# Optimization experiments

Measured on AMD Instinct MI355X. Metric: run time of the kernel, lower is better.

The kernel has to match this reference:

```python
import jax, jax.numpy as jnp
import numpy as np

B, T, D_IN, D_H, D_OUT = 32, 1024, 512, 1024, 512

def setup_inputs() -> dict:
    key = jax.random.key(0)
    kx, k1, k2, k3, k4, k5, k6 = jax.random.split(key, 7)
    # scale weights like typical init (1/sqrt(fan_in)) so sigmoid stays in a sane range
    x = jax.random.normal(kx, (B, T, D_IN), dtype=jnp.float32)
    Wh_w = jax.random.normal(k1, (D_H, D_H), dtype=jnp.float32) / np.sqrt(D_H)
    Wh_b = jax.random.normal(k2, (D_H,), dtype=jnp.float32) * 0.01
    Wx_w = jax.random.normal(k3, (D_H, D_IN), dtype=jnp.float32) / np.sqrt(D_IN)
    Wx_b = jax.random.normal(k4, (D_H,), dtype=jnp.float32) * 0.01
    Wy_w = jax.random.normal(k5, (D_OUT, D_H), dtype=jnp.float32) / np.sqrt(D_H)
    Wy_b = jax.random.normal(k6, (D_OUT,), dtype=jnp.float32) * 0.01
    return {"x": x, "Wh_w": Wh_w, "Wh_b": Wh_b, "Wx_w": Wx_w, "Wx_b": Wx_b,
            "Wy_w": Wy_w, "Wy_b": Wy_b}

def reference(x, Wh_w, Wh_b, Wx_w, Wx_b, Wy_w, Wy_b):
    # h_t = sigmoid(Wh h_{t-1} + b_h + Wx x_t + b_x); y_t = Wy h_t + b_y
    # Precompute input projection for all timesteps (one big GEMM).
    xp = jnp.einsum('bti,hi->bth', x, Wx_w) + Wx_b + Wh_b  # [B,T,H]
    xp_t = jnp.swapaxes(xp, 0, 1)  # [T,B,H] for scan
    h0 = jnp.zeros((x.shape[0], Wh_w.shape[0]), dtype=x.dtype)

    def step(h, xpt):
        h = jax.nn.sigmoid(h @ Wh_w.T + xpt)  # [B,H]
        y = h @ Wy_w.T + Wy_b                 # [B,O]
        return h, y

    _, ys = jax.lax.scan(step, h0, xp_t)  # ys: [T,B,O]
    return jnp.swapaxes(ys, 0, 1)  # [B,T,O]
```

## Files before the change

kernel.cpp:

```cpp
#include <hip/hip_runtime.h>

constexpr int Bb = 32;
constexpr int Tt = 1024;
constexpr int Hh = 1024;
constexpr int Di = 512;
constexpr int Do = 512;

using bf16x8 = __attribute__((ext_vector_type(8))) short;
using f32x4  = __attribute__((ext_vector_type(4))) float;

__device__ __forceinline__ f32x4 mfma16(bf16x8 a, bf16x8 b, f32x4 c) {
  return __builtin_amdgcn_mfma_f32_16x16x32_bf16(a, b, c, 0, 0, 0);
}
__device__ __forceinline__ unsigned short f2bf(float f) {
  unsigned u = __builtin_bit_cast(unsigned, f);
  u += 0x7FFFu + ((u >> 16) & 1u);
  return (unsigned short)(u >> 16);
}
__device__ __forceinline__ float bf2f(unsigned short h) {
  unsigned u = ((unsigned)h) << 16;
  return __builtin_bit_cast(float, u);
}

__device__ __forceinline__ void llc_store_u16(void* p, unsigned v) {
  asm volatile("global_store_short %0, %1, off sc0 sc1" :: "v"(p), "v"(v) : "memory");
}
__device__ __forceinline__ void llc_store_u32(void* p, unsigned v) {
  asm volatile("global_store_dword %0, %1, off sc0 sc1" :: "v"(p), "v"(v) : "memory");
}
__device__ __forceinline__ uint4 llc_load_flags(const void* p) {
  uint4 r;
  asm volatile("global_load_dwordx4 %0, %1, off sc0 sc1\n\ts_waitcnt vmcnt(0)"
               : "=v"(r) : "v"(p) : "memory");
  return r;
}

__global__ __launch_bounds__(256) void cvt4_kernel(const float* __restrict__ s,
                                                   unsigned short* __restrict__ d) {
  int i = (blockIdx.x * 256 + threadIdx.x) * 4;
  float4 v = *(const float4*)(s + i);
  ushort4 u = { f2bf(v.x), f2bf(v.y), f2bf(v.z), f2bf(v.w) };
  *(ushort4*)(d + i) = u;
}

template <int MODE>
__global__ __launch_bounds__(256)
void gemm_kernel(const void* __restrict__ Ap, const float* __restrict__ Bw,
                 const float* __restrict__ bias1, const float* __restrict__ bias2,
                 void* __restrict__ Cp) {
  constexpr int K = (MODE == 0) ? Di : Hh;
  constexpr int BM = 64, BN = 64, BK = 64;
  __shared__ unsigned short As[BM][80];
  __shared__ unsigned short Bs[BN][80];

  const int m0 = blockIdx.x * BM;
  const int n0 = blockIdx.y * BN;
  const int tid = threadIdx.x;
  const int lane = tid & 63;
  const int wave = tid >> 6;
  const int wm = (wave & 1) * 32;
  const int wn = (wave >> 1) * 32;
  const int fr = lane & 15;
  const int kg = lane >> 4;

  f32x4 acc[2][2] = {};

  const int srow = tid >> 2;
  const int scb  = (tid & 3) * 16;

  for (int k0 = 0; k0 < K; k0 += BK) {
    if constexpr (MODE == 0) {
      const float* a = (const float*)Ap + (size_t)(m0 + srow) * K + k0 + scb;
#pragma unroll
      for (int q = 0; q < 4; ++q) {
        float4 v = ((const float4*)a)[q];
        ushort4 u = { f2bf(v.x), f2bf(v.y), f2bf(v.z), f2bf(v.w) };
        *(ushort4*)&As[srow][scb + q * 4] = u;
      }
    } else {
      const unsigned short* a = (const unsigned short*)Ap + (size_t)(m0 + srow) * K + k0 + scb;
      *(uint4*)&As[srow][scb]     = ((const uint4*)a)[0];
      *(uint4*)&As[srow][scb + 8] = ((const uint4*)a)[1];
    }
    {
      const float* b = Bw + (size_t)(n0 + srow) * K + k0 + scb;
#pragma unroll
      for (int q = 0; q < 4; ++q) {
        float4 v = ((const float4*)b)[q];
        ushort4 u = { f2bf(v.x), f2bf(v.y), f2bf(v.z), f2bf(v.w) };
        *(ushort4*)&Bs[srow][scb + q * 4] = u;
      }
    }
    __syncthreads();

#pragma unroll
    for (int kk = 0; kk < 2; ++kk) {
      const int kb = kk * 32 + kg * 8;
      bf16x8 af[2], bf[2];
      af[0] = *(const bf16x8*)&As[wm + fr][kb];
      af[1] = *(const bf16x8*)&As[wm + 16 + fr][kb];
      bf[0] = *(const bf16x8*)&Bs[wn + fr][kb];
      bf[1] = *(const bf16x8*)&Bs[wn + 16 + fr][kb];
#pragma unroll
      for (int i = 0; i < 2; ++i)
#pragma unroll
        for (int j = 0; j < 2; ++j)
          acc[i][j] = mfma16(af[i], bf[j], acc[i][j]);
    }
    __syncthreads();
  }

#pragma unroll
  for (int i = 0; i < 2; ++i) {
#pragma unroll
    for (int j = 0; j < 2; ++j) {
      const int n = n0 + wn + j * 16 + fr;
      float bv;
      if constexpr (MODE == 0) bv = bias1[n] + bias2[n];
      else                     bv = bias1[n];
#pragma unroll
      for (int q = 0; q < 4; ++q) {
        const int m = m0 + wm + i * 16 + kg * 4 + q;
        float v = acc[i][j][q] + bv;
        if constexpr (MODE == 0) {
          int bb = m >> 10, ttt = m & 1023;
          ((unsigned short*)Cp)[((size_t)ttt * Bb + bb) * Hh + n] = f2bf(v);
        } else {
          int bb = m & 31, ttt = m >> 5;
          ((float*)Cp)[((size_t)bb * Tt + ttt) * Do + n] = v;
        }
      }
    }
  }
}

__global__ __launch_bounds__(512)
void scan_kernel(const unsigned short* __restrict__ Whb,
                 const unsigned short* __restrict__ xp,
                 unsigned short* __restrict__ hist,
                 unsigned short* __restrict__ hbuf,
                 unsigned* __restrict__ flags) {
  __shared__ unsigned short panel[16 * 1024];

  const int tid = threadIdx.x;
  const int g = blockIdx.x >> 3;
  const int r = blockIdx.x & 7;
  const int wave = tid >> 6;
  const int lane = tid & 63;
  const int nloc = lane & 15;
  const int kgrp = lane >> 4;
  const int hrow = r * 128 + wave * 16 + nloc;
  const int gb0 = g * 16;
  const int xmask = (nloc & 7) << 3;

  bf16x8 wf[32];
  {
    const unsigned short* wb = Whb + (size_t)hrow * Hh + kgrp * 8;
#pragma unroll
    for (int kk = 0; kk < 32; ++kk) wf[kk] = *(const bf16x8*)(wb + kk * 32);
#pragma unroll
    for (int kk = 0; kk < 32; ++kk) asm volatile("" : "+v"(wf[kk]));
  }

  unsigned* gflags = flags + g * 64;
  const int sb  = tid >> 5;
  const int sk0 = (tid & 31) * 32;

  for (int t = 0; t < Tt; ++t) {
    const int par = t & 1;
    const unsigned short* hsrc = hbuf + (size_t)par * Bb * Hh;
    unsigned short* hdst = hbuf + (size_t)(par ^ 1) * Bb * Hh;

    unsigned short xpv[4];
    const size_t xb = (size_t)t * Bb * Hh + hrow;
#pragma unroll
    for (int i = 0; i < 4; ++i) xpv[i] = xp[xb + (size_t)(gb0 + kgrp * 4 + i) * Hh];

    if (tid == 0) {
      for (;;) {
        uint4 f0 = llc_load_flags(gflags);
        uint4 f1 = llc_load_flags(gflags + 4);
        unsigned mn = f0.x;
        mn = mn < f0.y ? mn : f0.y;  mn = mn < f0.z ? mn : f0.z;  mn = mn < f0.w ? mn : f0.w;
        mn = mn < f1.x ? mn : f1.x;  mn = mn < f1.y ? mn : f1.y;
        mn = mn < f1.z ? mn : f1.z;  mn = mn < f1.w ? mn : f1.w;
        if (mn >= (unsigned)t) break;
      }
    }
    __syncthreads();

    {
      const unsigned* gsrc = (const unsigned*)(hsrc + (size_t)(gb0 + sb) * Hh + sk0);
      unsigned tmp[16];
#pragma unroll
      for (int q = 0; q < 16; ++q)
        tmp[q] = __hip_atomic_load(gsrc + q, __ATOMIC_RELAXED, __HIP_MEMORY_SCOPE_AGENT);
#pragma unroll
      for (int c = 0; c < 4; ++c) {
        uint4 v = { tmp[4 * c], tmp[4 * c + 1], tmp[4 * c + 2], tmp[4 * c + 3] };
        *(uint4*)&panel[sb * 1024 + ((sk0 + c * 8) ^ ((sb & 7) << 3))] = v;
      }
    }
    __syncthreads();

    f32x4 acc0 = {0.f, 0.f, 0.f, 0.f}, acc1 = {0.f, 0.f, 0.f, 0.f};
#pragma unroll
    for (int kk = 0; kk < 32; kk += 2) {
      bf16x8 a0 = *(const bf16x8*)&panel[nloc * 1024 + ((kk * 32 + kgrp * 8) ^ xmask)];
      bf16x8 a1 = *(const bf16x8*)&panel[nloc * 1024 + (((kk + 1) * 32 + kgrp * 8) ^ xmask)];
      acc0 = mfma16(a0, wf[kk], acc0);
      acc1 = mfma16(a1, wf[kk + 1], acc1);
    }
    f32x4 acc = acc0 + acc1;

    const size_t tb = (size_t)t * Bb * Hh;
#pragma unroll
    for (int i = 0; i < 4; ++i) {
      const int mb = gb0 + kgrp * 4 + i;
      float pre = acc[i] + bf2f(xpv[i]);
      float h = 1.0f / (1.0f + __expf(-pre));
      unsigned hb = f2bf(h);
      llc_store_u16(hdst + (size_t)mb * Hh + hrow, hb);
      hist[tb + (size_t)mb * Hh + hrow] = (unsigned short)hb;
    }

    asm volatile("s_waitcnt vmcnt(0)" ::: "memory");
    __syncthreads();
    if (tid == 0) llc_store_u32(gflags + r, (unsigned)(t + 1));
  }
}

extern "C" void kernel_launch(void* const* d_in, const int* in_sizes, int n_in,
                              void* d_out, int out_size, void* d_ws, size_t ws_size,
                              hipStream_t stream) {
  const float* x    = (const float*)d_in[0];
  const float* Wh_w = (const float*)d_in[1];
  const float* Wh_b = (const float*)d_in[2];
  const float* Wx_w = (const float*)d_in[3];
  const float* Wx_b = (const float*)d_in[4];
  const float* Wy_w = (const float*)d_in[5];
  const float* Wy_b = (const float*)d_in[6];

  char* ws = (char*)d_ws;
  constexpr size_t XP_OFF   = 0;
  constexpr size_t HIST_OFF = XP_OFF   + (size_t)Tt * Bb * Hh * 2;
  constexpr size_t WH_OFF   = HIST_OFF + (size_t)Tt * Bb * Hh * 2;
  constexpr size_t HBUF_OFF = WH_OFF   + (size_t)Hh * Hh * 2;
  constexpr size_t FLG_OFF  = HBUF_OFF + (size_t)2 * Bb * Hh * 2;

  unsigned short* xp   = (unsigned short*)(ws + XP_OFF);
  unsigned short* hist = (unsigned short*)(ws + HIST_OFF);
  unsigned short* whb  = (unsigned short*)(ws + WH_OFF);
  unsigned short* hbuf = (unsigned short*)(ws + HBUF_OFF);
  unsigned*       flags = (unsigned*)(ws + FLG_OFF);

  hipMemsetAsync(ws + HBUF_OFF, 0, (size_t)2 * Bb * Hh * 2 + 512, stream);

  cvt4_kernel<<<dim3((Hh * Hh) / (256 * 4)), dim3(256), 0, stream>>>(Wh_w, whb);

  gemm_kernel<0><<<dim3((Bb * Tt) / 64, Hh / 64), dim3(256), 0, stream>>>(
      (const void*)x, Wx_w, Wx_b, Wh_b, (void*)xp);

  {
    void* sargs[5] = { (void*)&whb, (void*)&xp, (void*)&hist, (void*)&hbuf, (void*)&flags };
    hipLaunchCooperativeKernel((const void*)scan_kernel, dim3(16), dim3(512), sargs, 0, stream);
  }

  gemm_kernel<1><<<dim3((Bb * Tt) / 64, Do / 64), dim3(256), 0, stream>>>(
      (const void*)hist, Wy_w, Wy_b, nullptr, d_out);
}
```

Baseline: 7.148 ms.

## Replace flag-based step barrier with per-element tagged hidden-state words

The scan kernel drops the separate per-group flag array, where one thread polled and then the block synchronised. Each hidden value is now stored as a 32-bit word holding the timestep tag in the high half and the bf16 value in the low half, in a triple-buffered array. Consumer threads poll their own 128-byte slice until every tag matches the expected step, then unpack the values into shared memory. This removes the producer-side vmcnt wait, a block barrier and the flag round trip from each step's critical path, at the cost of doubling the bytes moved per hidden-state exchange.

```diff
diff --git a/kernel.cpp b/kernel.cpp
--- a/kernel.cpp
+++ b/kernel.cpp
@@ -5,6 +5,7 @@
 constexpr int Hh = 1024;
 constexpr int Di = 512;
 constexpr int Do = 512;
+constexpr int TGSZ = Bb * Hh;
 
 using bf16x8 = __attribute__((ext_vector_type(8))) short;
 using f32x4  = __attribute__((ext_vector_type(4))) float;
@@ -20,19 +21,6 @@
 __device__ __forceinline__ float bf2f(unsigned short h) {
   unsigned u = ((unsigned)h) << 16;
   return __builtin_bit_cast(float, u);
-}
-
-__device__ __forceinline__ void llc_store_u16(void* p, unsigned v) {
-  asm volatile("global_store_short %0, %1, off sc0 sc1" :: "v"(p), "v"(v) : "memory");
-}
-__device__ __forceinline__ void llc_store_u32(void* p, unsigned v) {
-  asm volatile("global_store_dword %0, %1, off sc0 sc1" :: "v"(p), "v"(v) : "memory");
-}
-__device__ __forceinline__ uint4 llc_load_flags(const void* p) {
-  uint4 r;
-  asm volatile("global_load_dwordx4 %0, %1, off sc0 sc1\n\ts_waitcnt vmcnt(0)"
-               : "=v"(r) : "v"(p) : "memory");
-  return r;
 }
 
 __global__ __launch_bounds__(256) void cvt4_kernel(const float* __restrict__ s,
@@ -41,6 +29,11 @@
   float4 v = *(const float4*)(s + i);
   ushort4 u = { f2bf(v.x), f2bf(v.y), f2bf(v.z), f2bf(v.w) };
   *(ushort4*)(d + i) = u;
+}
+
+__global__ __launch_bounds__(256) void init_tags(unsigned* __restrict__ tg) {
+  int i = blockIdx.x * 256 + threadIdx.x;
+  tg[i] = (i < TGSZ) ? 0xFFFF0000u : 0xEEEE0000u;
 }
 
 template <int MODE>
@@ -96,16 +89,16 @@
 #pragma unroll
     for (int kk = 0; kk < 2; ++kk) {
       const int kb = kk * 32 + kg * 8;
-      bf16x8 af[2], bf[2];
-      af[0] = *(const bf16x8*)&As[wm + fr][kb];
-      af[1] = *(const bf16x8*)&As[wm + 16 + fr][kb];
-      bf[0] = *(const bf16x8*)&Bs[wn + fr][kb];
-      bf[1] = *(const bf16x8*)&Bs[wn + 16 + fr][kb];
+      bf16x8 af[2], bfr[2];
+      af[0]  = *(const bf16x8*)&As[wm + fr][kb];
+      af[1]  = *(const bf16x8*)&As[wm + 16 + fr][kb];
+      bfr[0] = *(const bf16x8*)&Bs[wn + fr][kb];
+      bfr[1] = *(const bf16x8*)&Bs[wn + 16 + fr][kb];
 #pragma unroll
       for (int i = 0; i < 2; ++i)
 #pragma unroll
         for (int j = 0; j < 2; ++j)
-          acc[i][j] = mfma16(af[i], bf[j], acc[i][j]);
+          acc[i][j] = mfma16(af[i], bfr[j], acc[i][j]);
     }
     __syncthreads();
   }
@@ -138,8 +131,7 @@
 void scan_kernel(const unsigned short* __restrict__ Whb,
                  const unsigned short* __restrict__ xp,
                  unsigned short* __restrict__ hist,
-                 unsigned short* __restrict__ hbuf,
-                 unsigned* __restrict__ flags) {
+                 unsigned* __restrict__ tg) {
   __shared__ unsigned short panel[16 * 1024];
 
   const int tid = threadIdx.x;
@@ -158,48 +150,63 @@
     const unsigned short* wb = Whb + (size_t)hrow * Hh + kgrp * 8;
 #pragma unroll
     for (int kk = 0; kk < 32; ++kk) wf[kk] = *(const bf16x8*)(wb + kk * 32);
-#pragma unroll
-    for (int kk = 0; kk < 32; ++kk) asm volatile("" : "+v"(wf[kk]));
-  }
-
-  unsigned* gflags = flags + g * 64;
-  const int sb  = tid >> 5;
-  const int sk0 = (tid & 31) * 32;
+  }
+
+  const int sb  = tid & 15;
+  const int kc  = tid >> 4;
+  const int sxs = (sb & 7) << 3;
 
   for (int t = 0; t < Tt; ++t) {
-    const int par = t & 1;
-    const unsigned short* hsrc = hbuf + (size_t)par * Bb * Hh;
-    unsigned short* hdst = hbuf + (size_t)(par ^ 1) * Bb * Hh;
+#pragma unroll
+    for (int kk = 0; kk < 32; kk += 8)
+      asm volatile("" : "+v"(wf[kk]), "+v"(wf[kk + 1]), "+v"(wf[kk + 2]), "+v"(wf[kk + 3]),
+                        "+v"(wf[kk + 4]), "+v"(wf[kk + 5]), "+v"(wf[kk + 6]), "+v"(wf[kk + 7]));
+
+    const int par = t % 3;
+    const int nxt = (t + 1) % 3;
 
     unsigned short xpv[4];
     const size_t xb = (size_t)t * Bb * Hh + hrow;
 #pragma unroll
     for (int i = 0; i < 4; ++i) xpv[i] = xp[xb + (size_t)(gb0 + kgrp * 4 + i) * Hh];
 
-    if (tid == 0) {
-      for (;;) {
-        uint4 f0 = llc_load_flags(gflags);
-        uint4 f1 = llc_load_flags(gflags + 4);
-        unsigned mn = f0.x;
-        mn = mn < f0.y ? mn : f0.y;  mn = mn < f0.z ? mn : f0.z;  mn = mn < f0.w ? mn : f0.w;
-        mn = mn < f1.x ? mn : f1.x;  mn = mn < f1.y ? mn : f1.y;
-        mn = mn < f1.z ? mn : f1.z;  mn = mn < f1.w ? mn : f1.w;
-        if (mn >= (unsigned)t) break;
-      }
-    }
-    __syncthreads();
+    const unsigned exp = ((unsigned)t - 1u) & 0xFFFFu;
+    const unsigned* src = tg + (size_t)par * TGSZ + (size_t)(gb0 + sb) * Hh + kc * 32;
+    uint4 d0, d1, d2, d3, d4, d5, d6, d7;
+    unsigned bad;
+    do {
+      asm volatile(
+          "global_load_dwordx4 %0, %8, off sc0 sc1\n\t"
+          "global_load_dwordx4 %1, %8, off offset:16 sc0 sc1\n\t"
+          "global_load_dwordx4 %2, %8, off offset:32 sc0 sc1\n\t"
+          "global_load_dwordx4 %3, %8, off offset:48 sc0 sc1\n\t"
+          "global_load_dwordx4 %4, %8, off offset:64 sc0 sc1\n\t"
+          "global_load_dwordx4 %5, %8, off offset:80 sc0 sc1\n\t"
+          "global_load_dwordx4 %6, %8, off offset:96 sc0 sc1\n\t"
+          "global_load_dwordx4 %7, %8, off offset:112 sc0 sc1\n\t"
+          "s_waitcnt vmcnt(0)"
+          : "=v"(d0), "=v"(d1), "=v"(d2), "=v"(d3),
+            "=v"(d4), "=v"(d5), "=v"(d6), "=v"(d7)
+          : "v"(src) : "memory");
+      bad = 0;
+#define CHK(v) bad |= ((v.x >> 16) ^ exp) | ((v.y >> 16) ^ exp) | \
+                      ((v.z >> 16) ^ exp) | ((v.w >> 16) ^ exp)
+      CHK(d0); CHK(d1); CHK(d2); CHK(d3); CHK(d4); CHK(d5); CHK(d6); CHK(d7);
+#undef CHK
+    } while (bad);
 
     {
-      const unsigned* gsrc = (const unsigned*)(hsrc + (size_t)(gb0 + sb) * Hh + sk0);
-      unsigned tmp[16];
-#pragma unroll
-      for (int q = 0; q < 16; ++q)
-        tmp[q] = __hip_atomic_load(gsrc + q, __ATOMIC_RELAXED, __HIP_MEMORY_SCOPE_AGENT);
-#pragma unroll
-      for (int c = 0; c < 4; ++c) {
-        uint4 v = { tmp[4 * c], tmp[4 * c + 1], tmp[4 * c + 2], tmp[4 * c + 3] };
-        *(uint4*)&panel[sb * 1024 + ((sk0 + c * 8) ^ ((sb & 7) << 3))] = v;
-      }
+#define PK(a, b) (((a) & 0xFFFFu) | ((b) << 16))
+      uint4 p0 = { PK(d0.x, d0.y), PK(d0.z, d0.w), PK(d1.x, d1.y), PK(d1.z, d1.w) };
+      uint4 p1 = { PK(d2.x, d2.y), PK(d2.z, d2.w), PK(d3.x, d3.y), PK(d3.z, d3.w) };
+      uint4 p2 = { PK(d4.x, d4.y), PK(d4.z, d4.w), PK(d5.x, d5.y), PK(d5.z, d5.w) };
+      uint4 p3 = { PK(d6.x, d6.y), PK(d6.z, d6.w), PK(d7.x, d7.y), PK(d7.z, d7.w) };
+#undef PK
+      const int pb = sb * 1024, k0 = kc * 32;
+      *(uint4*)&panel[pb + ((k0)      ^ sxs)] = p0;
+      *(uint4*)&panel[pb + ((k0 + 8)  ^ sxs)] = p1;
+      *(uint4*)&panel[pb + ((k0 + 16) ^ sxs)] = p2;
+      *(uint4*)&panel[pb + ((k0 + 24) ^ sxs)] = p3;
     }
     __syncthreads();
 
@@ -214,19 +221,20 @@
     f32x4 acc = acc0 + acc1;
 
     const size_t tb = (size_t)t * Bb * Hh;
+    unsigned* dbase = tg + (size_t)nxt * TGSZ + hrow;
 #pragma unroll
     for (int i = 0; i < 4; ++i) {
       const int mb = gb0 + kgrp * 4 + i;
       float pre = acc[i] + bf2f(xpv[i]);
       float h = 1.0f / (1.0f + __expf(-pre));
-      unsigned hb = f2bf(h);
-      llc_store_u16(hdst + (size_t)mb * Hh + hrow, hb);
-      hist[tb + (size_t)mb * Hh + hrow] = (unsigned short)hb;
-    }
-
-    asm volatile("s_waitcnt vmcnt(0)" ::: "memory");
-    __syncthreads();
-    if (tid == 0) llc_store_u32(gflags + r, (unsigned)(t + 1));
+      unsigned short hb = f2bf(h);
+      unsigned word = ((unsigned)t << 16) | (unsigned)hb;
+      asm volatile("global_store_dword %0, %1, off sc0 sc1"
+                   :: "v"(dbase + (size_t)mb * Hh), "v"(word) : "memory");
+      hist[tb + (size_t)mb * Hh + hrow] = hb;
+    }
+
+    __syncthreads();
   }
 }
 
@@ -245,16 +253,14 @@
   constexpr size_t XP_OFF   = 0;
   constexpr size_t HIST_OFF = XP_OFF   + (size_t)Tt * Bb * Hh * 2;
   constexpr size_t WH_OFF   = HIST_OFF + (size_t)Tt * Bb * Hh * 2;
-  constexpr size_t HBUF_OFF = WH_OFF   + (size_t)Hh * Hh * 2;
-  constexpr size_t FLG_OFF  = HBUF_OFF + (size_t)2 * Bb * Hh * 2;
+  constexpr size_t TG_OFF   = WH_OFF   + (size_t)Hh * Hh * 2;
 
   unsigned short* xp   = (unsigned short*)(ws + XP_OFF);
   unsigned short* hist = (unsigned short*)(ws + HIST_OFF);
   unsigned short* whb  = (unsigned short*)(ws + WH_OFF);
-  unsigned short* hbuf = (unsigned short*)(ws + HBUF_OFF);
-  unsigned*       flags = (unsigned*)(ws + FLG_OFF);
-
-  hipMemsetAsync(ws + HBUF_OFF, 0, (size_t)2 * Bb * Hh * 2 + 512, stream);
+  unsigned*       tg   = (unsigned*)(ws + TG_OFF);
+
+  init_tags<<<dim3((3 * TGSZ) / 256), dim3(256), 0, stream>>>(tg);
 
   cvt4_kernel<<<dim3((Hh * Hh) / (256 * 4)), dim3(256), 0, stream>>>(Wh_w, whb);
 
@@ -262,7 +268,7 @@
       (const void*)x, Wx_w, Wx_b, Wh_b, (void*)xp);
 
   {
-    void* sargs[5] = { (void*)&whb, (void*)&xp, (void*)&hist, (void*)&hbuf, (void*)&flags };
+    void* sargs[4] = { (void*)&whb, (void*)&xp, (void*)&hist, (void*)&tg };
     hipLaunchCooperativeKernel((const void*)scan_kernel, dim3(16), dim3(512), sargs, 0, stream);
   }
 
```

After: 5.938 ms. 16.9% less time.
